# Optimization experiments

Hardware: AMD Instinct MI355X
Metric: run time of the kernel (lower is better)

Reference implementation:

```python
import jax, jax.numpy as jnp
import numpy as np

N_HEAD = 16
D_MODEL = 1024
# c_attn compression metadata (coeff_ratio=0.25, 'medium')
ATTN_N = D_MODEL * 3 * D_MODEL          # 3145728
ATTN_PAD = 4194304                       # next pow2
ATTN_FFT = ATTN_PAD // 2 + 1             # 2097153
ATTN_KEEP = int(ATTN_FFT * 0.25)         # 524288
PROJ_N = D_MODEL * D_MODEL               # 1048576 (already pow2)
PROJ_PAD = PROJ_N
PROJ_FFT = PROJ_PAD // 2 + 1             # 524289
PROJ_KEEP = int(PROJ_FFT * 0.25)         # 131072


def setup_inputs() -> dict:
    key = jax.random.key(0)
    ks = jax.random.split(key, 9)
    B, S = 2, 2048
    x = jax.random.normal(ks[0], (B, S, D_MODEL), dtype=jnp.float32)
    c_attn_re = jax.random.normal(ks[1], (ATTN_KEEP,), dtype=jnp.float32)
    c_attn_im = jax.random.normal(ks[2], (ATTN_KEEP,), dtype=jnp.float32)
    # indices from topk are unique -> use a random permutation prefix
    c_attn_idx = jax.random.permutation(ks[3], ATTN_FFT)[:ATTN_KEEP].astype(jnp.int32)
    c_attn_scale = jnp.ones((1,), dtype=jnp.float32)
    c_proj_re = jax.random.normal(ks[4], (PROJ_KEEP,), dtype=jnp.float32)
    c_proj_im = jax.random.normal(ks[5], (PROJ_KEEP,), dtype=jnp.float32)
    c_proj_idx = jax.random.permutation(ks[6], PROJ_FFT)[:PROJ_KEEP].astype(jnp.int32)
    c_proj_scale = jnp.ones((1,), dtype=jnp.float32)
    c_attn_bias = jax.random.normal(ks[7], (3 * D_MODEL,), dtype=jnp.float32)
    c_proj_bias = jax.random.normal(ks[8], (D_MODEL,), dtype=jnp.float32)
    return dict(x=x, c_attn_re=c_attn_re, c_attn_im=c_attn_im, c_attn_idx=c_attn_idx,
                c_attn_scale=c_attn_scale, c_proj_re=c_proj_re, c_proj_im=c_proj_im,
                c_proj_idx=c_proj_idx, c_proj_scale=c_proj_scale,
                c_attn_bias=c_attn_bias, c_proj_bias=c_proj_bias)


def _decompress(re, im, idx, fft_len, pad_n, n, shape, scale):
    # zero-init + scatter of kept complex coeffs, then inverse rFFT
    full = jnp.zeros((fft_len,), dtype=jnp.complex64).at[idx].set(re + 1j * im)
    restored = jnp.fft.irfft(full, n=pad_n)[:n]
    return restored.reshape(shape) * scale[0]


def reference(x, c_attn_re, c_attn_im, c_attn_idx, c_attn_scale,
              c_proj_re, c_proj_im, c_proj_idx, c_proj_scale,
              c_attn_bias, c_proj_bias):
    Wa = _decompress(c_attn_re, c_attn_im, c_attn_idx, ATTN_FFT, ATTN_PAD,
                     ATTN_N, (D_MODEL, 3 * D_MODEL), c_attn_scale)
    Wp = _decompress(c_proj_re, c_proj_im, c_proj_idx, PROJ_FFT, PROJ_PAD,
                     PROJ_N, (D_MODEL, D_MODEL), c_proj_scale)
    B, S, _ = x.shape
    hd = D_MODEL // N_HEAD
    # F.linear(x, W.T, b) == x @ W + b  (Conv1D convention)
    qkv = x @ Wa + c_attn_bias                       # [B,S,3D]
    q, k, v = jnp.split(qkv, 3, axis=2)
    def heads(t):  # [B,S,D] -> [B,H,S,hd]
        return t.reshape(B, S, N_HEAD, hd).transpose(0, 2, 1, 3)
    q, k, v = heads(q), heads(k), heads(v)
    scores = jnp.einsum('bhqd,bhkd->bhqk', q, k) / jnp.sqrt(jnp.float32(hd))
    attn = jax.nn.softmax(scores, axis=-1)           # dropout = identity (eval)
    out = jnp.einsum('bhqk,bhkd->bhqd', attn, v)
    out = out.transpose(0, 2, 1, 3).reshape(B, S, D_MODEL)
    return out @ Wp + c_proj_bias
```

## Files before the change

### kernel.cpp

```cpp
#include <hip/hip_runtime.h>
#include <math.h>

#define N_HEADC  16
#define D_MODELC 1024
#define ATTN_N_C    3145728
#define ATTN_PAD_C  4194304
#define ATTN_NC     2097152
#define ATTN_KEEP_C 524288
#define PROJ_N_C    1048576
#define PROJ_PAD_C  1048576
#define PROJ_NC     524288
#define PROJ_KEEP_C 131072
#define BATCH_C 2
#define SEQ_C   2048

#define CEXP_C 0.18033688011112042f

typedef __attribute__((ext_vector_type(8))) short s16x8;
typedef __attribute__((ext_vector_type(4))) float f32x4;

#define AS1U(p) ((const __attribute__((address_space(1))) uint*)(p))
#define AS3U(p) ((__attribute__((address_space(3))) uint*)(p))

static __device__ __forceinline__ ushort f2bf(float f) {
    __bf16 b = (__bf16)f;
    return __builtin_bit_cast(ushort, b);
}
static __device__ __forceinline__ float bf2f(ushort u) {
    return __builtin_bit_cast(float, ((uint)u) << 16);
}
static __device__ __forceinline__ float2 cmul(float2 a, float2 b) {
    return make_float2(a.x * b.x - a.y * b.y, a.x * b.y + a.y * b.x);
}
static __device__ __forceinline__ float2 cadd(float2 a, float2 b) {
    return make_float2(a.x + b.x, a.y + b.y);
}
static __device__ __forceinline__ float2 csub(float2 a, float2 b) {
    return make_float2(a.x - b.x, a.y - b.y);
}
static __device__ __forceinline__ float2 crot(float2 z) {
    return make_float2(-z.y, z.x);
}

static __device__ __forceinline__ void r8core(const float2* a, float2* B) {
    const float2 t0 = cadd(a[0], a[4]), t1 = csub(a[0], a[4]);
    const float2 t2 = cadd(a[2], a[6]), t3 = csub(a[2], a[6]);
    const float2 t4 = cadd(a[1], a[5]), t5 = csub(a[1], a[5]);
    const float2 t6 = cadd(a[3], a[7]), t7 = csub(a[3], a[7]);
    const float2 E0 = cadd(t0, t2), E2 = csub(t0, t2);
    const float2 E1 = cadd(t1, crot(t3)), E3 = csub(t1, crot(t3));
    const float2 F0 = cadd(t4, t6), F2 = csub(t4, t6);
    const float2 F1 = cadd(t5, crot(t7)), F3 = csub(t5, crot(t7));
    const float c = 0.70710678118654752f;
    const float2 G1 = make_float2(c * (F1.x - F1.y), c * (F1.x + F1.y));
    const float2 G2 = crot(F2);
    const float2 G3 = make_float2(c * (-F3.x - F3.y), c * (F3.x - F3.y));
    B[0] = cadd(E0, F0); B[4] = csub(E0, F0);
    B[1] = cadd(E1, G1); B[5] = csub(E1, G1);
    B[2] = cadd(E2, G2); B[6] = csub(E2, G2);
    B[3] = cadd(E3, G3); B[7] = csub(E3, G3);
}


static __device__ __forceinline__ float2 pack_eval(
    const float2* __restrict__ H, int Nc, float th0, int k) {
    float2 g = H[k];
    float2 hm = H[Nc - k];
    if (k == 0) { g.y = 0.f; hm.y = 0.f; }
    float2 gh = make_float2(hm.x, -hm.y);
    float2 sum = make_float2(g.x + gh.x, g.y + gh.y);
    float2 dif = make_float2(g.x - gh.x, g.y - gh.y);
    float si, co;
    __sincosf(th0 * (float)k, &si, &co);
    float2 t = make_float2(dif.x * co - dif.y * si, dif.x * si + dif.y * co);
    return make_float2(sum.x - t.y, sum.y + t.x);
}

static __device__ __forceinline__ void r2_body(
    const float2* __restrict__ in, float2* __restrict__ out,
    int slog, int m, int half, int t) {
    if (t >= half) return;
    int s = 1 << slog;
    int q = t & (s - 1);
    int p = t >> slog;
    float si, co;
    __sincosf((float)(M_PI / (double)m) * (float)p, &si, &co);
    float2 a = in[q + s * p];
    float2 b = in[q + s * (p + m)];
    float2 su = cadd(a, b);
    float2 di = csub(a, b);
    int ob = q + ((s << 1) * p);
    out[ob]     = su;
    out[ob + s] = make_float2(di.x * co - di.y * si, di.x * si + di.y * co);
}

static __device__ __forceinline__ void r2_pack_body(
    const float2* __restrict__ H, float2* __restrict__ out,
    int Nc, float th0, int m, int half, int t) {
    if (t >= half) return;
    float2 a = pack_eval(H, Nc, th0, t);
    float2 b = pack_eval(H, Nc, th0, t + m);
    float si, co;
    __sincosf((float)(M_PI / (double)m) * (float)t, &si, &co);
    float2 su = cadd(a, b);
    float2 di = csub(a, b);
    out[2 * t]     = su;
    out[2 * t + 1] = make_float2(di.x * co - di.y * si, di.x * si + di.y * co);
}

static __device__ __forceinline__ void r8_body(
    const float2* __restrict__ in, float2* __restrict__ out,
    int slog, int M, float ang0, int eighth, int t) {
    if (t >= eighth) return;
    const int s = 1 << slog;
    const int q = t & (s - 1);
    const int p = t >> slog;
    float2 a[8];
#pragma unroll
    for (int j = 0; j < 8; ++j)
        a[j] = in[q + (size_t)s * (p + j * M)];
    float2 B[8];
    r8core(a, B);
    float si, co;
    __sincosf(ang0 * (float)p, &si, &co);
    const float2 w = make_float2(co, si);
    const int ob = q + 8 * s * p;
    out[ob] = B[0];
    float2 wj = w;
    out[ob + s] = cmul(wj, B[1]);
#pragma unroll
    for (int j = 2; j < 8; ++j) {
        wj = cmul(wj, w);
        out[ob + j * s] = cmul(wj, B[j]);
    }
}

static __device__ void r64_body(
    float2 (*Ysh)[8][9],
    const float2* __restrict__ in, float2* __restrict__ out,
    int slog, int M, int vb) {
    const int tid = threadIdx.x;
    const int g = tid & 31, u = tid >> 5;
    const int s = 1 << slog;
    const int M8 = M >> 3;
    const int G = vb * 32 + g;
    const int q = G & (s - 1);
    const int p0 = G >> slog;

    const int p = p0 + u * M8;
    float2 a[8];
#pragma unroll
    for (int j = 0; j < 8; ++j)
        a[j] = in[q + (size_t)s * (p + j * M)];
    float2 B[8];
    r8core(a, B);
    float si, co;
    __sincosf((0.78539816339744831f / (float)M) * (float)p, &si, &co);
    const float2 w = make_float2(co, si);
    Ysh[g][u][0] = B[0];
    float2 wj = w;
    Ysh[g][u][1] = cmul(wj, B[1]);
#pragma unroll
    for (int j = 2; j < 8; ++j) {
        wj = cmul(wj, w);
        Ysh[g][u][j] = cmul(wj, B[j]);
    }
    __syncthreads();

    float2 z[8];
#pragma unroll
    for (int jp = 0; jp < 8; ++jp)
        z[jp] = Ysh[g][jp][u];
    float2 B2[8];
    r8core(z, B2);
    __sincosf((0.78539816339744831f / (float)M8) * (float)p0, &si, &co);
    const float2 w2 = make_float2(co, si);
    const size_t ob = (size_t)q + (size_t)u * s + (size_t)64 * s * p0;
    out[ob] = B2[0];
    float2 wj2 = w2;
    out[ob + (size_t)8 * s] = cmul(wj2, B2[1]);
#pragma unroll
    for (int j2 = 2; j2 < 8; ++j2) {
        wj2 = cmul(wj2, w2);
        out[ob + (size_t)j2 * 8 * s] = cmul(wj2, B2[j2]);
    }
}

static __device__ void r64_pack_body(
    float2 (*Ysh)[8][9],
    const float2* __restrict__ H, float2* __restrict__ out,
    int Nc, float th0, int M, int vb) {
    const int tid = threadIdx.x;
    const int g = tid & 31, u = tid >> 5;
    const int M8 = M >> 3;
    const int p0 = vb * 32 + g;
    const int p = p0 + u * M8;
    float2 a[8];
#pragma unroll
    for (int j = 0; j < 8; ++j)
        a[j] = pack_eval(H, Nc, th0, p + j * M);
    float2 B[8];
    r8core(a, B);
    float si, co;
    __sincosf((0.78539816339744831f / (float)M) * (float)p, &si, &co);
    const float2 w = make_float2(co, si);
    Ysh[g][u][0] = B[0];
    float2 wj = w;
    Ysh[g][u][1] = cmul(wj, B[1]);
#pragma unroll
    for (int j = 2; j < 8; ++j) {
        wj = cmul(wj, w);
        Ysh[g][u][j] = cmul(wj, B[j]);
    }
    __syncthreads();

    float2 z[8];
#pragma unroll
    for (int jp = 0; jp < 8; ++jp)
        z[jp] = Ysh[g][jp][u];
    float2 B2[8];
    r8core(z, B2);
    __sincosf((0.78539816339744831f / (float)M8) * (float)p0, &si, &co);
    const float2 w2 = make_float2(co, si);
    const size_t ob = (size_t)u + (size_t)64 * p0;
    out[ob] = B2[0];
    float2 wj2 = w2;
    out[ob + 8] = cmul(wj2, B2[1]);
#pragma unroll
    for (int j2 = 2; j2 < 8; ++j2) {
        wj2 = cmul(wj2, w2);
        out[ob + (size_t)j2 * 8] = cmul(wj2, B2[j2]);
    }
}

static __device__ __forceinline__ void transpose_body(
    float (*T)[33], const float2* __restrict__ z, ushort* __restrict__ WT,
    int Kd, int Nd, float inv, const float* __restrict__ sc, int qcols, int vb) {
    const int nbx = Nd >> 5;
    const int n0 = (vb % nbx) * 32, k0 = (vb / nbx) * 32;
    const int tx = threadIdx.x & 31, ty = threadIdx.x >> 5;
    const float s = inv * sc[0];
    for (int r = ty; r < 32; r += 8) {
        size_t j = (size_t)(k0 + r) * Nd + n0 + tx;
        float2 zz = z[j >> 1];
        T[r][tx] = (j & 1) ? zz.y : zz.x;
    }
    __syncthreads();
    for (int r = ty; r < 32; r += 8) {
        const float fs = ((n0 + r) < qcols) ? s * CEXP_C : s;
        WT[(size_t)(n0 + r) * Kd + k0 + tx] = f2bf(T[tx][r] * fs);
    }
}


__global__ __launch_bounds__(256) void x_scatter(
    const float* __restrict__ x, ushort* __restrict__ xb,
    const float* __restrict__ re_a, const float* __restrict__ im_a,
    const int* __restrict__ idx_a, float2* __restrict__ Ha,
    const float* __restrict__ re_p, const float* __restrict__ im_p,
    const int* __restrict__ idx_p, float2* __restrict__ Hp) {
    const int B = blockIdx.x;
    if (B < 4096) {
        const int i = B * 256 + threadIdx.x;
        float4 v = *(const float4*)(x + (size_t)i * 4);
        ushort4 o;
        o.x = f2bf(v.x); o.y = f2bf(v.y); o.z = f2bf(v.z); o.w = f2bf(v.w);
        *(ushort4*)(xb + (size_t)i * 4) = o;
    } else {
        const int t = (B - 4096) * 256 + threadIdx.x;
        if (t < ATTN_KEEP_C) {
            Ha[idx_a[t]] = make_float2(re_a[t], im_a[t]);
        } else {
            const int u = t - ATTN_KEEP_C;
            Hp[idx_p[u]] = make_float2(re_p[u], im_p[u]);
        }
    }
}

__global__ __launch_bounds__(256) void fft_pack1(
    const float2* __restrict__ Ha, float2* __restrict__ oa, float tha, int na,
    const float2* __restrict__ Hp, float2* __restrict__ op, float thp,
    int mp, int halfp) {
    __shared__ float2 Ysh[32][8][9];
    if ((int)blockIdx.x < na)
        r64_pack_body(Ysh, Ha, oa, ATTN_NC, tha, ATTN_NC >> 3, blockIdx.x);
    else
        r2_pack_body(Hp, op, PROJ_NC, thp, mp, halfp,
                     (blockIdx.x - na) * 256 + threadIdx.x);
}

__global__ __launch_bounds__(256) void fft_r64_dual(
    const float2* __restrict__ ia, float2* __restrict__ oa, int sla, int Ma, int na,
    const float2* __restrict__ ip, float2* __restrict__ op, int slp, int Mp) {
    __shared__ float2 Ysh[32][8][9];
    if ((int)blockIdx.x < na)
        r64_body(Ysh, ia, oa, sla, Ma, blockIdx.x);
    else
        r64_body(Ysh, ip, op, slp, Mp, blockIdx.x - na);
}

__global__ __launch_bounds__(256) void fft_r8_r64(
    const float2* __restrict__ ia, float2* __restrict__ oa, int sla, float ang0,
    int eighth, int na,
    const float2* __restrict__ ip, float2* __restrict__ op, int slp, int Mp) {
    __shared__ float2 Ysh[32][8][9];
    if ((int)blockIdx.x < na)
        r8_body(ia, oa, sla, 1, ang0, eighth, (blockIdx.x) * 256 + threadIdx.x);
    else
        r64_body(Ysh, ip, op, slp, Mp, blockIdx.x - na);
}

__global__ __launch_bounds__(256) void transpose_dual(
    const float2* __restrict__ za, ushort* __restrict__ Wa, const float* __restrict__ sca,
    const float2* __restrict__ zp, ushort* __restrict__ Wp, const float* __restrict__ scp) {
    __shared__ float T[32][33];
    if (blockIdx.x < 3072)
        transpose_body(T, za, Wa, 1024, 3072, 1.f / ATTN_PAD_C, sca, 1024, blockIdx.x);
    else
        transpose_body(T, zp, Wp, 1024, 1024, 1.f / PROJ_PAD_C, scp, 0, blockIdx.x - 3072);
}

template <int OUTMODE>
__global__ __launch_bounds__(256) void gemm_bt_mfma(
    const ushort* __restrict__ A, const ushort* __restrict__ Bt,
    const float* __restrict__ bias, void* __restrict__ Cout,
    ushort* __restrict__ Vt, int M, int N, int K) {
    __shared__ ushort As[128 * 64];
    __shared__ ushort Bs[128 * 64];
    const int tid = threadIdx.x;
    const int wid = tid >> 6, lane = tid & 63, quad = lane >> 4, l16 = lane & 15;
    const int row0 = blockIdx.y * 128, col0 = blockIdx.x * 128;
    const int mh = (wid >> 1) * 64, nh = (wid & 1) * 64;
    const int r7 = l16 & 7;

    f32x4 acc[4][4] = {};

    for (int k0 = 0; k0 < K; k0 += 64) {
        __syncthreads();
#pragma unroll
        for (int rep = 0; rep < 4; ++rep) {
            int c = tid + rep * 256;
            int r = c >> 3;
            int kc = (c & 7) ^ (r & 7);
            ushort* lbA = &As[(rep * 256 + wid * 64) * 8];
            ushort* lbB = &Bs[(rep * 256 + wid * 64) * 8];
            __builtin_amdgcn_global_load_lds(
                AS1U(A + (size_t)(row0 + r) * K + k0 + kc * 8), AS3U(lbA), 16, 0, 0);
            __builtin_amdgcn_global_load_lds(
                AS1U(Bt + (size_t)(col0 + r) * K + k0 + kc * 8), AS3U(lbB), 16, 0, 0);
        }
        __syncthreads();
#pragma unroll
        for (int kk = 0; kk < 2; ++kk) {
            const int slot = ((kk * 4 + quad) ^ r7) * 8;
            s16x8 af[4], bfr[4];
#pragma unroll
            for (int mi = 0; mi < 4; ++mi)
                af[mi] = *(const s16x8*)&As[(mh + mi * 16 + l16) * 64 + slot];
#pragma unroll
            for (int ni = 0; ni < 4; ++ni)
                bfr[ni] = *(const s16x8*)&Bs[(nh + ni * 16 + l16) * 64 + slot];
#pragma unroll
            for (int mi = 0; mi < 4; ++mi)
#pragma unroll
                for (int ni = 0; ni < 4; ++ni)
                    acc[mi][ni] = __builtin_amdgcn_mfma_f32_16x16x32_bf16(
                        af[mi], bfr[ni], acc[mi][ni], 0, 0, 0);
        }
    }

#pragma unroll
    for (int mi = 0; mi < 4; ++mi)
#pragma unroll
        for (int ni = 0; ni < 4; ++ni) {
            const int col = col0 + nh + ni * 16 + l16;
            const int rbase = row0 + mh + mi * 16 + quad * 4;
            float bv = bias[col];
            if (OUTMODE == 1 && col < 1024) bv *= CEXP_C;
            if (OUTMODE == 0) {
                float* C = (float*)Cout;
#pragma unroll
                for (int j = 0; j < 4; ++j)
                    C[(size_t)(rbase + j) * N + col] = acc[mi][ni][j] + bv;
            } else {
                if (col < 2048) {
                    ushort* C = (ushort*)Cout;
#pragma unroll
                    for (int j = 0; j < 4; ++j)
                        C[(size_t)(rbase + j) * N + col] = f2bf(acc[mi][ni][j] + bv);
                } else {
                    const int bb = rbase >> 11;
                    const int seq = rbase & 2047;
                    const int d = col - 2048;
                    ushort4 pk;
                    pk.x = f2bf(acc[mi][ni][0] + bv);
                    pk.y = f2bf(acc[mi][ni][1] + bv);
                    pk.z = f2bf(acc[mi][ni][2] + bv);
                    pk.w = f2bf(acc[mi][ni][3] + bv);
                    *(ushort4*)&Vt[(size_t)bb * 2097152 + (size_t)d * 2048 + seq] = pk;
                }
            }
        }
}

__global__ __launch_bounds__(512, 4) void attn_fwd_mfma(
    const ushort* __restrict__ qkv, const ushort* __restrict__ Vt,
    ushort* __restrict__ ctx) {
    const int L = blockIdx.x;
    const int xcd = L & 7, slot = L >> 3;
    const int g = xcd * 4 + (slot >> 4);
    const int qb = slot & 15;
    const int b = g >> 4, h = g & 15;
    const int tid = threadIdx.x;
    const int wid = tid >> 6, lane = tid & 63, quad = lane >> 4, l16 = lane & 15;
    const int wq = wid * 16;
    const int r7 = l16 & 7;

    __shared__ ushort Ks[2][64 * 64];
    __shared__ ushort Vts[2][64 * 64];
    __shared__ ushort Ps[128 * 64];

#pragma unroll
    for (int rep = 0; rep < 2; ++rep) {
        int c = tid + rep * 512;
        int r = c >> 3;
        int kc = (c & 7) ^ (r & 7);
        ushort* lb = &Ps[(rep * 512 + wid * 64) * 8];
        __builtin_amdgcn_global_load_lds(
            AS1U(qkv + (size_t)(b * 2048 + qb * 128 + r) * 3072 + h * 64 + kc * 8),
            AS3U(lb), 16, 0, 0);
    }
    __syncthreads();

    s16x8 qreg[2];
#pragma unroll
    for (int ks = 0; ks < 2; ++ks) {
        const int slot2 = ((ks * 4 + quad) ^ r7) * 8;
        qreg[ks] = *(const s16x8*)&Ps[(wq + l16) * 64 + slot2];
    }

    f32x4 o[4] = {};
    float l_r = 0.f;

    for (int tt = 0; tt < 32; tt += 2) {
        __syncthreads();
#pragma unroll
        for (int half = 0; half < 2; ++half) {
            const int kt = tt + half;
            int r = tid >> 3;
            int kc = (tid & 7) ^ (r & 7);
            ushort* lbK = &Ks[half][(wid * 64) * 8];
            ushort* lbV = &Vts[half][(wid * 64) * 8];
            __builtin_amdgcn_global_load_lds(
                AS1U(qkv + (size_t)(b * 2048 + kt * 64 + r) * 3072 + 1024 + h * 64 + kc * 8),
                AS3U(lbK), 16, 0, 0);
            __builtin_amdgcn_global_load_lds(
                AS1U(Vt + (size_t)b * 2097152 + (size_t)(h * 64 + r) * 2048 + kt * 64 + kc * 8),
                AS3U(lbV), 16, 0, 0);
        }
        __syncthreads();

#pragma unroll
        for (int half = 0; half < 2; ++half) {
            f32x4 s[4] = {};
            __builtin_amdgcn_s_setprio(1);
#pragma unroll
            for (int ks = 0; ks < 2; ++ks) {
                const int slot2 = ((ks * 4 + quad) ^ r7) * 8;
                s16x8 ka[4];
#pragma unroll
                for (int mi = 0; mi < 4; ++mi)
                    ka[mi] = *(const s16x8*)&Ks[half][(mi * 16 + l16) * 64 + slot2];
#pragma unroll
                for (int mi = 0; mi < 4; ++mi)
                    s[mi] = __builtin_amdgcn_mfma_f32_16x16x32_bf16(
                        ka[mi], qreg[ks], s[mi], 0, 0, 0);
            }
            __builtin_amdgcn_s_setprio(0);

#pragma unroll
            for (int mi = 0; mi < 4; ++mi) {
                ushort4 pk;
#pragma unroll
                for (int j = 0; j < 4; ++j) {
                    float p = exp2f(s[mi][j]);
                    l_r += p;
                    ((ushort*)&pk)[j] = f2bf(p);
                }
                const int jq = 2 * mi + (quad >> 1);
                *(ushort4*)&Ps[(wq + l16) * 64 + ((jq ^ r7)) * 8 + (quad & 1) * 4] = pk;
            }

            __builtin_amdgcn_s_setprio(1);
#pragma unroll
            for (int ks = 0; ks < 2; ++ks) {
                const int slot2 = ((ks * 4 + quad) ^ r7) * 8;
                s16x8 va[4], pb;
#pragma unroll
                for (int md = 0; md < 4; ++md)
                    va[md] = *(const s16x8*)&Vts[half][(md * 16 + l16) * 64 + slot2];
                pb = *(const s16x8*)&Ps[(wq + l16) * 64 + slot2];
#pragma unroll
                for (int md = 0; md < 4; ++md)
                    o[md] = __builtin_amdgcn_mfma_f32_16x16x32_bf16(
                        va[md], pb, o[md], 0, 0, 0);
            }
            __builtin_amdgcn_s_setprio(0);
        }
    }

    float l = l_r;
    l += __shfl_xor(l, 16);
    l += __shfl_xor(l, 32);
    const float inv = 1.f / l;
    const size_t row = (size_t)(b * 2048 + qb * 128 + wq + l16);
#pragma unroll
    for (int md = 0; md < 4; ++md) {
        ushort4 pk;
#pragma unroll
        for (int j = 0; j < 4; ++j)
            ((ushort*)&pk)[j] = f2bf(o[md][j] * inv);
        *(ushort4*)&ctx[row * 1024 + h * 64 + md * 16 + quad * 4] = pk;
    }
}

extern "C" void kernel_launch(void* const* d_in, const int* in_sizes, int n_in,
                              void* d_out, int out_size, void* d_ws, size_t ws_size,
                              hipStream_t stream) {
    const float* x        = (const float*)d_in[0];
    const float* attn_re  = (const float*)d_in[1];
    const float* attn_im  = (const float*)d_in[2];
    const int*   attn_idx = (const int*)d_in[3];
    const float* attn_sc  = (const float*)d_in[4];
    const float* proj_re  = (const float*)d_in[5];
    const float* proj_im  = (const float*)d_in[6];
    const int*   proj_idx = (const int*)d_in[7];
    const float* proj_sc  = (const float*)d_in[8];
    const float* attn_b   = (const float*)d_in[9];
    const float* proj_b   = (const float*)d_in[10];
    float* out = (float*)d_out;

    const size_t MB = 1048576;
    char* w = (char*)d_ws;
    float2* A0  = (float2*)(w);
    float2* A1  = (float2*)(w + 16 * MB);
    float2* Ha  = (float2*)(w + 32 * MB);
    float2* Hp  = (float2*)(w + 49 * MB);
    float2* P0  = (float2*)(w + 54 * MB);
    float2* P1  = (float2*)(w + 58 * MB);
    ushort* WaT = (ushort*)(w + 62 * MB);
    ushort* WpT = (ushort*)(w + 68 * MB);
    ushort* x_bf= (ushort*)(w + 70 * MB);
    ushort* qkvb= (ushort*)(w);
    ushort* Vt  = (ushort*)(w + 24 * MB);
    ushort* ctx = (ushort*)(w + 32 * MB);

    hipMemsetAsync(w + 32 * MB, 0, 22 * MB, stream);

    x_scatter<<<6656, 256, 0, stream>>>(
        x, x_bf, attn_re, attn_im, attn_idx, Ha, proj_re, proj_im, proj_idx, Hp);

    fft_pack1<<<2048, 256, 0, stream>>>(
        Ha, A1, (float)(2.0 * M_PI / ATTN_PAD_C), 1024,
        Hp, P1, (float)(2.0 * M_PI / PROJ_PAD_C), PROJ_NC / 2, PROJ_NC / 2);

    fft_r64_dual<<<1280, 256, 0, stream>>>(A1, A0, 6,  ATTN_NC >> 9,  1024,
                                           P1, P0, 1,  PROJ_NC >> 4);
    fft_r64_dual<<<1280, 256, 0, stream>>>(A0, A1, 12, ATTN_NC >> 15, 1024,
                                           P0, P1, 7,  PROJ_NC >> 10);
    fft_r8_r64 <<<1280, 256, 0, stream>>>(A1, A0, 18, (float)(M_PI / 4.0),
                                          ATTN_NC / 8, 1024,
                                          P1, P0, 13, PROJ_NC >> 16);
    transpose_dual<<<4096, 256, 0, stream>>>(A0, WaT, attn_sc, P0, WpT, proj_sc);

    gemm_bt_mfma<1><<<dim3(3072 / 128, 4096 / 128), 256, 0, stream>>>(
        x_bf, WaT, attn_b, qkvb, Vt, 4096, 3072, 1024);

    attn_fwd_mfma<<<512, 512, 0, stream>>>(qkvb, Vt, ctx);

    gemm_bt_mfma<0><<<dim3(1024 / 128, 4096 / 128), 256, 0, stream>>>(
        ctx, WpT, proj_b, out, (ushort*)nullptr, 4096, 1024, 1024);
}
```

Before: 260.8 us.

## Software-pipeline K/V tile loads in attention with a prefetch distance of two

The attention kernel used to load two K/V tiles into LDS and then compute on both, so every load was exposed. It now preloads tiles 0 and 1 in the prologue. Each iteration computes one tile and then, after a barrier, issues the global-to-LDS load for tile tt+2 into the buffer just freed. This lets the next tile's data arrive while the following tile is being computed. Correctness depends on the barrier waiting for outstanding LDS-direct loads before the other buffer is read.

```diff
diff --git a/kernel.cpp b/kernel.cpp
--- a/kernel.cpp
+++ b/kernel.cpp
@@ -420,6 +420,9 @@
     __shared__ ushort Vts[2][64 * 64];
     __shared__ ushort Ps[128 * 64];
 
+    const int sr = tid >> 3;
+    const int skc = (tid & 7) ^ (sr & 7);
+
 #pragma unroll
     for (int rep = 0; rep < 2; ++rep) {
         int c = tid + rep * 512;
@@ -430,6 +433,17 @@
             AS1U(qkv + (size_t)(b * 2048 + qb * 128 + r) * 3072 + h * 64 + kc * 8),
             AS3U(lb), 16, 0, 0);
     }
+#pragma unroll
+    for (int kt = 0; kt < 2; ++kt) {
+        ushort* lbK = &Ks[kt][(wid * 64) * 8];
+        ushort* lbV = &Vts[kt][(wid * 64) * 8];
+        __builtin_amdgcn_global_load_lds(
+            AS1U(qkv + (size_t)(b * 2048 + kt * 64 + sr) * 3072 + 1024 + h * 64 + skc * 8),
+            AS3U(lbK), 16, 0, 0);
+        __builtin_amdgcn_global_load_lds(
+            AS1U(Vt + (size_t)b * 2097152 + (size_t)(h * 64 + sr) * 2048 + kt * 64 + skc * 8),
+            AS3U(lbV), 16, 0, 0);
+    }
     __syncthreads();
 
     s16x8 qreg[2];
@@ -442,70 +456,66 @@
     f32x4 o[4] = {};
     float l_r = 0.f;
 
-    for (int tt = 0; tt < 32; tt += 2) {
+    for (int tt = 0; tt < 32; ++tt) {
+        const int buf = tt & 1;
+
+        f32x4 s[4] = {};
+        __builtin_amdgcn_s_setprio(1);
+#pragma unroll
+        for (int ks = 0; ks < 2; ++ks) {
+            const int slot2 = ((ks * 4 + quad) ^ r7) * 8;
+            s16x8 ka[4];
+#pragma unroll
+            for (int mi = 0; mi < 4; ++mi)
+                ka[mi] = *(const s16x8*)&Ks[buf][(mi * 16 + l16) * 64 + slot2];
+#pragma unroll
+            for (int mi = 0; mi < 4; ++mi)
+                s[mi] = __builtin_amdgcn_mfma_f32_16x16x32_bf16(
+                    ka[mi], qreg[ks], s[mi], 0, 0, 0);
+        }
+        __builtin_amdgcn_s_setprio(0);
+
+#pragma unroll
+        for (int mi = 0; mi < 4; ++mi) {
+            ushort4 pk;
+#pragma unroll
+            for (int j = 0; j < 4; ++j) {
+                float p = exp2f(s[mi][j]);
+                l_r += p;
+                ((ushort*)&pk)[j] = f2bf(p);
+            }
+            const int jq = 2 * mi + (quad >> 1);
+            *(ushort4*)&Ps[(wq + l16) * 64 + ((jq ^ r7)) * 8 + (quad & 1) * 4] = pk;
+        }
+
+        __builtin_amdgcn_s_setprio(1);
+#pragma unroll
+        for (int ks = 0; ks < 2; ++ks) {
+            const int slot2 = ((ks * 4 + quad) ^ r7) * 8;
+            s16x8 va[4], pb;
+#pragma unroll
+            for (int md = 0; md < 4; ++md)
+                va[md] = *(const s16x8*)&Vts[buf][(md * 16 + l16) * 64 + slot2];
+            pb = *(const s16x8*)&Ps[(wq + l16) * 64 + slot2];
+#pragma unroll
+            for (int md = 0; md < 4; ++md)
+                o[md] = __builtin_amdgcn_mfma_f32_16x16x32_bf16(
+                    va[md], pb, o[md], 0, 0, 0);
+        }
+        __builtin_amdgcn_s_setprio(0);
+
         __syncthreads();
-#pragma unroll
-        for (int half = 0; half < 2; ++half) {
-            const int kt = tt + half;
-            int r = tid >> 3;
-            int kc = (tid & 7) ^ (r & 7);
-            ushort* lbK = &Ks[half][(wid * 64) * 8];
-            ushort* lbV = &Vts[half][(wid * 64) * 8];
+
+        if (tt + 2 < 32) {
+            const int kt = tt + 2;
+            ushort* lbK = &Ks[buf][(wid * 64) * 8];
+            ushort* lbV = &Vts[buf][(wid * 64) * 8];
             __builtin_amdgcn_global_load_lds(
-                AS1U(qkv + (size_t)(b * 2048 + kt * 64 + r) * 3072 + 1024 + h * 64 + kc * 8),
+                AS1U(qkv + (size_t)(b * 2048 + kt * 64 + sr) * 3072 + 1024 + h * 64 + skc * 8),
                 AS3U(lbK), 16, 0, 0);
             __builtin_amdgcn_global_load_lds(
-                AS1U(Vt + (size_t)b * 2097152 + (size_t)(h * 64 + r) * 2048 + kt * 64 + kc * 8),
+                AS1U(Vt + (size_t)b * 2097152 + (size_t)(h * 64 + sr) * 2048 + kt * 64 + skc * 8),
                 AS3U(lbV), 16, 0, 0);
-        }
-        __syncthreads();
-
-#pragma unroll
-        for (int half = 0; half < 2; ++half) {
-            f32x4 s[4] = {};
-            __builtin_amdgcn_s_setprio(1);
-#pragma unroll
-            for (int ks = 0; ks < 2; ++ks) {
-                const int slot2 = ((ks * 4 + quad) ^ r7) * 8;
-                s16x8 ka[4];
-#pragma unroll
-                for (int mi = 0; mi < 4; ++mi)
-                    ka[mi] = *(const s16x8*)&Ks[half][(mi * 16 + l16) * 64 + slot2];
-#pragma unroll
-                for (int mi = 0; mi < 4; ++mi)
-                    s[mi] = __builtin_amdgcn_mfma_f32_16x16x32_bf16(
-                        ka[mi], qreg[ks], s[mi], 0, 0, 0);
-            }
-            __builtin_amdgcn_s_setprio(0);
-
-#pragma unroll
-            for (int mi = 0; mi < 4; ++mi) {
-                ushort4 pk;
-#pragma unroll
-                for (int j = 0; j < 4; ++j) {
-                    float p = exp2f(s[mi][j]);
-                    l_r += p;
-                    ((ushort*)&pk)[j] = f2bf(p);
-                }
-                const int jq = 2 * mi + (quad >> 1);
-                *(ushort4*)&Ps[(wq + l16) * 64 + ((jq ^ r7)) * 8 + (quad & 1) * 4] = pk;
-            }
-
-            __builtin_amdgcn_s_setprio(1);
-#pragma unroll
-            for (int ks = 0; ks < 2; ++ks) {
-                const int slot2 = ((ks * 4 + quad) ^ r7) * 8;
-                s16x8 va[4], pb;
-#pragma unroll
-                for (int md = 0; md < 4; ++md)
-                    va[md] = *(const s16x8*)&Vts[half][(md * 16 + l16) * 64 + slot2];
-                pb = *(const s16x8*)&Ps[(wq + l16) * 64 + slot2];
-#pragma unroll
-                for (int md = 0; md < 4; ++md)
-                    o[md] = __builtin_amdgcn_mfma_f32_16x16x32_bf16(
-                        va[md], pb, o[md], 0, 0, 0);
-            }
-            __builtin_amdgcn_s_setprio(0);
         }
     }
 
```

After: 260.0 us. About the same (-0.3%).
